# Optimization experiments

Measured on AMD Instinct MI355X. Metric: run time of the kernel, lower is better.

The kernel has to match this reference:

```python
import jax, jax.numpy as jnp
import numpy as np

B, S, D_IN, D_OUT = 64, 2048, 256, 256  # batch, doc_len, doc_hidden_dim, 2*hidden_dim


def setup_inputs() -> dict:
    key = jax.random.key(0)
    k1, k2, k3, k4 = jax.random.split(key, 4)
    doc_encoding = jax.random.normal(k1, (B, S, D_IN), dtype=jnp.float32)
    score_soft = jax.random.uniform(k2, (2, B, S), dtype=jnp.float32)
    # gold spans: sort along axis 0 so answer_idx[0] <= answer_idx[1]
    answer_idx = jnp.sort(jax.random.randint(k3, (2, B), 0, S), axis=0)
    W_mlp = jax.random.normal(k4, (D_IN, D_OUT), dtype=jnp.float32) * 0.05
    b_mlp = jnp.zeros((D_OUT,), dtype=jnp.float32)
    return {"doc_encoding": doc_encoding, "score_soft": score_soft,
            "answer_idx": answer_idx, "W_mlp": W_mlp, "b_mlp": b_mlp}


def _span_sum(doc_proj, s_idx, e_idx):
    # masked segment-sum over ragged spans [s_idx, e_idx]; empty (s>e) -> zeros
    pos = jnp.arange(doc_proj.shape[1])  # [S]
    mask = ((pos[None, :] >= s_idx[:, None]) & (pos[None, :] <= e_idx[:, None]))
    return jnp.einsum('bs,bsd->bd', mask.astype(doc_proj.dtype), doc_proj)


def reference(doc_encoding, score_soft, answer_idx, W_mlp, b_mlp):
    # MLP_QQ projection: [B,S,D_IN] -> [B,S,D_OUT]
    doc_proj = jnp.einsum('bsd,de->bse', doc_encoding, W_mlp) + b_mlp
    # hard span: argmax of start/end scores (zeros when start > end, handled by empty mask)
    s_idx = jnp.argmax(score_soft[0], axis=-1)
    e_idx = jnp.argmax(score_soft[1], axis=-1)
    answer_encoding = _span_sum(doc_proj, s_idx, e_idx)
    # teacher-forcing span: gold start/end indices
    answer_encoding_gold = _span_sum(doc_proj, answer_idx[0], answer_idx[1])
    return (answer_encoding, answer_encoding_gold)
```

## Files before the change

kernel.cpp:

```cpp
#include <hip/hip_runtime.h>

#define S_LEN 2048
#define D 256
#define BATCH 64
#define CHUNK 64

__global__ void argmax_kernel(const float* __restrict__ score,
                              int* __restrict__ out_idx) {
    const int row = blockIdx.x;
    const float* p = score + (size_t)row * S_LEN;
    const int t = threadIdx.x;

    float best = -INFINITY;
    int bidx = 0x7fffffff;
    for (int i = t; i < S_LEN; i += 256) {
        float v = p[i];
        if (v > best) { best = v; bidx = i; }
    }

    __shared__ float sval[256];
    __shared__ int   sidx[256];
    sval[t] = best; sidx[t] = bidx;
    __syncthreads();
    for (int off = 128; off > 0; off >>= 1) {
        if (t < off) {
            float v2 = sval[t + off]; int i2 = sidx[t + off];
            if (v2 > sval[t] || (v2 == sval[t] && i2 < sidx[t])) {
                sval[t] = v2; sidx[t] = i2;
            }
        }
        __syncthreads();
    }
    if (t == 0) out_idx[row] = sidx[0];
}

__global__ void spansum_kernel(const float* __restrict__ doc,
                               const int* __restrict__ hard_idx,
                               const int* __restrict__ answer_idx,
                               float* __restrict__ acc) {
    const int r = blockIdx.y;
    const int b = r & 63;
    int lo, hi;
    if (r < 64) { lo = hard_idx[b];   hi = hard_idx[64 + b]; }
    else        { lo = answer_idx[b]; hi = answer_idx[64 + b]; }

    const int c0 = blockIdx.x * CHUNK;
    const int s0 = max(lo, c0);
    const int s1 = min(hi + 1, c0 + CHUNK);
    if (s0 >= s1) return;

    const int t    = threadIdx.x;
    const int wave = t >> 6;
    const int lane = t & 63;

    const float* base = doc + (size_t)b * S_LEN * D + lane * 4;
    float4 sum = make_float4(0.f, 0.f, 0.f, 0.f);
    int s = s0 + wave;
    for (; s + 4 < s1; s += 8) {
        float4 v0 = *reinterpret_cast<const float4*>(base + (size_t)s * D);
        float4 v1 = *reinterpret_cast<const float4*>(base + (size_t)(s + 4) * D);
        sum.x += v0.x + v1.x; sum.y += v0.y + v1.y;
        sum.z += v0.z + v1.z; sum.w += v0.w + v1.w;
    }
    if (s < s1) {
        float4 v0 = *reinterpret_cast<const float4*>(base + (size_t)s * D);
        sum.x += v0.x; sum.y += v0.y; sum.z += v0.z; sum.w += v0.w;
    }

    __shared__ float lds[4][D];
    *reinterpret_cast<float4*>(&lds[wave][lane * 4]) = sum;
    __syncthreads();

    float tot = lds[0][t] + lds[1][t] + lds[2][t] + lds[3][t];
    atomicAdd(&acc[(size_t)r * D + t], tot);
}

__global__ void mlp_kernel(const float* __restrict__ acc,
                           const int* __restrict__ hard_idx,
                           const int* __restrict__ answer_idx,
                           const float* __restrict__ W,
                           const float* __restrict__ bvec,
                           float* __restrict__ out) {
    const int r = blockIdx.x;
    const int b = r & 63;
    int lo, hi;
    if (r < 64) { lo = hard_idx[b];   hi = hard_idx[64 + b]; }
    else        { lo = answer_idx[b]; hi = answer_idx[64 + b]; }
    const float cnt = (hi >= lo) ? (float)(hi - lo + 1) : 0.0f;

    const int t = threadIdx.x;
    __shared__ float av[D];
    av[t] = acc[(size_t)r * D + t];
    __syncthreads();

    float sum = cnt * bvec[t];
#pragma unroll 8
    for (int k = 0; k < D; ++k) {
        sum += av[k] * W[(size_t)k * D + t];
    }
    out[(size_t)r * D + t] = sum;
}

extern "C" void kernel_launch(void* const* d_in, const int* in_sizes, int n_in,
                              void* d_out, int out_size, void* d_ws, size_t ws_size,
                              hipStream_t stream) {
    const float* doc        = (const float*)d_in[0];
    const float* score      = (const float*)d_in[1];
    const int*   answer_idx = (const int*)  d_in[2];
    const float* W          = (const float*)d_in[3];
    const float* bvec       = (const float*)d_in[4];
    float*       out        = (float*)d_out;

    int*   hard_idx = (int*)d_ws;
    float* acc      = (float*)((char*)d_ws + 1024);

    hipMemsetAsync(acc, 0, (size_t)2 * BATCH * D * sizeof(float), stream);

    argmax_kernel<<<dim3(2 * BATCH), dim3(256), 0, stream>>>(score, hard_idx);

    dim3 g2(S_LEN / CHUNK, 2 * BATCH);
    spansum_kernel<<<g2, dim3(256), 0, stream>>>(doc, hard_idx, answer_idx, acc);

    mlp_kernel<<<dim3(2 * BATCH), dim3(256), 0, stream>>>(acc, hard_idx, answer_idx,
                                                          W, bvec, out);
}
```

Measured before the change: 209.2 us.

## Fuse argmax into span-sum kernel and replace atomics with per-chunk partials

After: 203.5 us. 2.7% less time.

```diff
diff --git a/kernel.cpp b/kernel.cpp
--- a/kernel.cpp
+++ b/kernel.cpp
@@ -4,96 +4,108 @@
 #define D 256
 #define BATCH 64
 #define CHUNK 64
+#define NCHUNK (S_LEN / CHUNK)
 
-__global__ void argmax_kernel(const float* __restrict__ score,
-                              int* __restrict__ out_idx) {
-    const int row = blockIdx.x;
-    const float* p = score + (size_t)row * S_LEN;
-    const int t = threadIdx.x;
+__global__ void spansum_fused_kernel(const float* __restrict__ doc,
+                                     const float* __restrict__ score,
+                                     const int* __restrict__ answer_idx,
+                                     float* __restrict__ acc_part,
+                                     int* __restrict__ cnt_part) {
+    const int chunk = blockIdx.x;
+    const int r     = blockIdx.y;
+    const int b     = r & 63;
+    const int t     = threadIdx.x;
 
-    float best = -INFINITY;
-    int bidx = 0x7fffffff;
-    for (int i = t; i < S_LEN; i += 256) {
-        float v = p[i];
-        if (v > best) { best = v; bidx = i; }
+    __shared__ float sv0[256]; __shared__ int si0[256];
+    __shared__ float sv1[256]; __shared__ int si1[256];
+    __shared__ float lds[4][D];
+
+    int lo, hi;
+    if (r < 64) {
+        const float4* p0 = reinterpret_cast<const float4*>(score + (size_t)b * S_LEN);
+        const float4* p1 = reinterpret_cast<const float4*>(score + (size_t)(64 + b) * S_LEN);
+        const float4 a0 = p0[2 * t], b0 = p0[2 * t + 1];
+        const float4 a1 = p1[2 * t], b1 = p1[2 * t + 1];
+        const float v0[8] = {a0.x, a0.y, a0.z, a0.w, b0.x, b0.y, b0.z, b0.w};
+        const float v1[8] = {a1.x, a1.y, a1.z, a1.w, b1.x, b1.y, b1.z, b1.w};
+        float best0 = v0[0]; int idx0 = 8 * t;
+        float best1 = v1[0]; int idx1 = 8 * t;
+#pragma unroll
+        for (int j = 1; j < 8; ++j) {
+            if (v0[j] > best0) { best0 = v0[j]; idx0 = 8 * t + j; }
+            if (v1[j] > best1) { best1 = v1[j]; idx1 = 8 * t + j; }
+        }
+        sv0[t] = best0; si0[t] = idx0;
+        sv1[t] = best1; si1[t] = idx1;
+        __syncthreads();
+        for (int off = 128; off > 0; off >>= 1) {
+            if (t < off) {
+                float v; int i;
+                v = sv0[t + off]; i = si0[t + off];
+                if (v > sv0[t] || (v == sv0[t] && i < si0[t])) { sv0[t] = v; si0[t] = i; }
+                v = sv1[t + off]; i = si1[t + off];
+                if (v > sv1[t] || (v == sv1[t] && i < si1[t])) { sv1[t] = v; si1[t] = i; }
+            }
+            __syncthreads();
+        }
+        lo = si0[0]; hi = si1[0];
+    } else {
+        lo = answer_idx[b]; hi = answer_idx[64 + b];
     }
 
-    __shared__ float sval[256];
-    __shared__ int   sidx[256];
-    sval[t] = best; sidx[t] = bidx;
-    __syncthreads();
-    for (int off = 128; off > 0; off >>= 1) {
-        if (t < off) {
-            float v2 = sval[t + off]; int i2 = sidx[t + off];
-            if (v2 > sval[t] || (v2 == sval[t] && i2 < sidx[t])) {
-                sval[t] = v2; sidx[t] = i2;
-            }
-        }
-        __syncthreads();
-    }
-    if (t == 0) out_idx[row] = sidx[0];
-}
-
-__global__ void spansum_kernel(const float* __restrict__ doc,
-                               const int* __restrict__ hard_idx,
-                               const int* __restrict__ answer_idx,
-                               float* __restrict__ acc) {
-    const int r = blockIdx.y;
-    const int b = r & 63;
-    int lo, hi;
-    if (r < 64) { lo = hard_idx[b];   hi = hard_idx[64 + b]; }
-    else        { lo = answer_idx[b]; hi = answer_idx[64 + b]; }
-
-    const int c0 = blockIdx.x * CHUNK;
+    const int c0 = chunk * CHUNK;
     const int s0 = max(lo, c0);
     const int s1 = min(hi + 1, c0 + CHUNK);
-    if (s0 >= s1) return;
 
-    const int t    = threadIdx.x;
     const int wave = t >> 6;
     const int lane = t & 63;
 
-    const float* base = doc + (size_t)b * S_LEN * D + lane * 4;
     float4 sum = make_float4(0.f, 0.f, 0.f, 0.f);
-    int s = s0 + wave;
-    for (; s + 4 < s1; s += 8) {
-        float4 v0 = *reinterpret_cast<const float4*>(base + (size_t)s * D);
-        float4 v1 = *reinterpret_cast<const float4*>(base + (size_t)(s + 4) * D);
-        sum.x += v0.x + v1.x; sum.y += v0.y + v1.y;
-        sum.z += v0.z + v1.z; sum.w += v0.w + v1.w;
-    }
-    if (s < s1) {
-        float4 v0 = *reinterpret_cast<const float4*>(base + (size_t)s * D);
-        sum.x += v0.x; sum.y += v0.y; sum.z += v0.z; sum.w += v0.w;
+    if (s0 < s1) {
+        const float* base = doc + (size_t)b * S_LEN * D + lane * 4;
+        int s = s0 + wave;
+        for (; s + 4 < s1; s += 8) {
+            float4 u0 = *reinterpret_cast<const float4*>(base + (size_t)s * D);
+            float4 u1 = *reinterpret_cast<const float4*>(base + (size_t)(s + 4) * D);
+            sum.x += u0.x + u1.x; sum.y += u0.y + u1.y;
+            sum.z += u0.z + u1.z; sum.w += u0.w + u1.w;
+        }
+        if (s < s1) {
+            float4 u0 = *reinterpret_cast<const float4*>(base + (size_t)s * D);
+            sum.x += u0.x; sum.y += u0.y; sum.z += u0.z; sum.w += u0.w;
+        }
     }
 
-    __shared__ float lds[4][D];
     *reinterpret_cast<float4*>(&lds[wave][lane * 4]) = sum;
     __syncthreads();
 
-    float tot = lds[0][t] + lds[1][t] + lds[2][t] + lds[3][t];
-    atomicAdd(&acc[(size_t)r * D + t], tot);
+    const float tot = lds[0][t] + lds[1][t] + lds[2][t] + lds[3][t];
+    acc_part[((size_t)r * NCHUNK + chunk) * D + t] = tot;
+    if (t == 0) cnt_part[r * NCHUNK + chunk] = (s1 > s0) ? (s1 - s0) : 0;
 }
 
-__global__ void mlp_kernel(const float* __restrict__ acc,
-                           const int* __restrict__ hard_idx,
-                           const int* __restrict__ answer_idx,
+__global__ void mlp_kernel(const float* __restrict__ acc_part,
+                           const int* __restrict__ cnt_part,
                            const float* __restrict__ W,
                            const float* __restrict__ bvec,
                            float* __restrict__ out) {
     const int r = blockIdx.x;
-    const int b = r & 63;
-    int lo, hi;
-    if (r < 64) { lo = hard_idx[b];   hi = hard_idx[64 + b]; }
-    else        { lo = answer_idx[b]; hi = answer_idx[64 + b]; }
-    const float cnt = (hi >= lo) ? (float)(hi - lo + 1) : 0.0f;
+    const int t = threadIdx.x;
 
-    const int t = threadIdx.x;
     __shared__ float av[D];
-    av[t] = acc[(size_t)r * D + t];
+    float s = 0.0f;
+#pragma unroll 4
+    for (int c = 0; c < NCHUNK; ++c)
+        s += acc_part[((size_t)r * NCHUNK + c) * D + t];
+    av[t] = s;
+
+    int cnt = 0;
+#pragma unroll 4
+    for (int c = 0; c < NCHUNK; ++c)
+        cnt += cnt_part[r * NCHUNK + c];
     __syncthreads();
 
-    float sum = cnt * bvec[t];
+    float sum = (float)cnt * bvec[t];
 #pragma unroll 8
     for (int k = 0; k < D; ++k) {
         sum += av[k] * W[(size_t)k * D + t];
@@ -111,16 +123,13 @@
     const float* bvec       = (const float*)d_in[4];
     float*       out        = (float*)d_out;
 
-    int*   hard_idx = (int*)d_ws;
-    float* acc      = (float*)((char*)d_ws + 1024);
+    float* acc_part = (float*)d_ws;
+    int*   cnt_part = (int*)((char*)d_ws + (size_t)128 * NCHUNK * D * sizeof(float));
 
-    hipMemsetAsync(acc, 0, (size_t)2 * BATCH * D * sizeof(float), stream);
+    dim3 g1(NCHUNK, 2 * BATCH);
+    spansum_fused_kernel<<<g1, dim3(256), 0, stream>>>(doc, score, answer_idx,
+                                                       acc_part, cnt_part);
 
-    argmax_kernel<<<dim3(2 * BATCH), dim3(256), 0, stream>>>(score, hard_idx);
-
-    dim3 g2(S_LEN / CHUNK, 2 * BATCH);
-    spansum_kernel<<<g2, dim3(256), 0, stream>>>(doc, hard_idx, answer_idx, acc);
-
-    mlp_kernel<<<dim3(2 * BATCH), dim3(256), 0, stream>>>(acc, hard_idx, answer_idx,
+    mlp_kernel<<<dim3(2 * BATCH), dim3(256), 0, stream>>>(acc_part, cnt_part,
                                                           W, bvec, out);
 }
```
